# Performance work log

Hardware: AMD Instinct MI355X
Metric: run time of the kernel (lower is better)

The kernel has to match this reference:

```python
import jax, jax.numpy as jnp
import numpy as np

B, K, D = 2048, 100000, 50  # batch, memory-bank size (num users), USER_VEC_DIM

def setup_inputs() -> dict:
    key = jax.random.key(0)
    k1, k2 = jax.random.split(key)
    x = jax.random.normal(k1, (B, D), dtype=jnp.float32)   # batch of user vectors
    M = jax.random.normal(k2, (K, D), dtype=jnp.float32)   # user_memory_vec bank
    return {"x": x, "M": M}

def reference(x, M):
    # Batched form of the per-item Python loop in call():
    #   mu = M @ u ; gamma = softmax(mu, axis=0) ; u_ = sum_k gamma_k * M[k]
    scores = jnp.einsum('bd,kd->bk', x, M)           # [B, K]
    attn = jax.nn.softmax(scores, axis=-1)           # softmax over memory slots
    u_ = jnp.einsum('bk,kd->bd', attn, M)            # attention readout [B, D]
    return jnp.concatenate([x, u_], axis=-1)         # [B, 2D]
```

## Files before the change

kernel.cpp:

```cpp
#include <hip/hip_runtime.h>
#include <hip/hip_bf16.h>
#include <math.h>

#define B_SZ 2048
#define K_SZ 100000
#define D_SZ 50
#define BT   64
#define CK   64
#define STR  72
#define MTS  78
#define SHIFT 30.0f
#define LOG2E 1.4426950408889634f
#define SHIFT_L2 43.280851226668905f
#define PSTRIDE 52
#define NCH   1563
#define IMG_CH 9216
#define IMG_BYTES ((size_t)NCH * IMG_CH * 2)
#define NSEG  18
#define PART_BYTES ((size_t)B_SZ * PSTRIDE * sizeof(float))

typedef short short8 __attribute__((ext_vector_type(8)));
typedef short short4v __attribute__((ext_vector_type(4)));
typedef float f32x4 __attribute__((ext_vector_type(4)));

#if __has_builtin(__builtin_amdgcn_mfma_f32_16x16x16bf16_1k)
#define HAVE_BF16_K16 1
#else
#define HAVE_BF16_K16 0
#endif

__device__ __forceinline__ unsigned short bf16_rne(float f) {
    union { float f; unsigned int u; } v; v.f = f;
    unsigned int r = (v.u + 0x7fffu + ((v.u >> 16) & 1u)) >> 16;
    return (unsigned short)r;
}
__device__ __forceinline__ float bf16_to_f(unsigned short h) {
    union { unsigned int u; float f; } v; v.u = ((unsigned int)h) << 16;
    return v.f;
}

__device__ __forceinline__ void load_lds16(const void* g, void* l) {
    __builtin_amdgcn_global_load_lds(
        (const __attribute__((address_space(1))) unsigned int*)g,
        (__attribute__((address_space(3))) unsigned int*)l, 16, 0, 0);
}

__global__ __launch_bounds__(256)
void precompute_m(const float* __restrict__ M, unsigned short* __restrict__ img) {
    __shared__ __align__(16) unsigned short Mt[64 * MTS];
    const int t = threadIdx.x;
    const int c0 = blockIdx.x;
    const int k0 = c0 * 64;
    for (int i = t; i < (64 * MTS) / 2; i += 256) ((unsigned int*)Mt)[i] = 0;
    __syncthreads();
    unsigned int* gh = (unsigned int*)(img + (size_t)c0 * IMG_CH);
    for (int i = t; i < 64 * 36; i += 256) {
        int r = i / 36, cd = i - r * 36, c = cd * 2;
        int kg = k0 + r;
        unsigned int val = 0;
        if (kg < K_SZ && c < D_SZ) {
            float2 v = *(const float2*)&M[(size_t)kg * D_SZ + c];
            val = ((unsigned int)bf16_rne(v.y) << 16) | bf16_rne(v.x);
            Mt[c * MTS + r]       = (unsigned short)(val & 0xffffu);
            Mt[(c + 1) * MTS + r] = (unsigned short)(val >> 16);
        }
        gh[i] = val;
    }
    __syncthreads();
    unsigned int* gt = (unsigned int*)(img + (size_t)c0 * IMG_CH + 64 * STR);
    for (int i = t; i < 64 * 36; i += 256) {
        int r = i / 36, c = i - r * 36;
        gt[i] = *(const unsigned int*)&Mt[r * MTS + c * 2];
    }
}

__global__ __launch_bounds__(512, 4)
void attend_fast(const float* __restrict__ x, const unsigned short* __restrict__ img,
                 float* __restrict__ part, int slice) {
    __shared__ __align__(16) unsigned short lds[2 * IMG_CH];
    __shared__ float lsc[4][64];

    const int t = threadIdx.x;
    const int w = t >> 6, lane = t & 63;
    const int quad = lane >> 4, lq = lane & 15;

    const int bid = blockIdx.x;
    const int rr = bid >> 3;
    const int split = (rr >> 5) * 8 + (bid & 7);
    const int xtile = rr & 31;
    const int b0 = xtile * BT;
    const int kbeg = split * slice;
    const int kend = min(kbeg + slice, K_SZ);

    const int nt0 = (w & 1) * 2;
    const int mblk = w >> 1;

    short8 xh[2][2], xl[2][2];
    for (int j = 0; j < 2; ++j) {
        int row = b0 + (nt0 + j) * 16 + lq;
        const float* xr = x + (size_t)row * D_SZ;
        for (int ki = 0; ki < 2; ++ki) {
            int d0 = ki * 32 + quad * 8;
            float v[8];
#pragma unroll
            for (int e = 0; e < 8; ++e) v[e] = 0.f;
            if (d0 + 8 <= D_SZ) {
#pragma unroll
                for (int e = 0; e < 4; ++e) {
                    float2 f2 = *(const float2*)&xr[d0 + 2 * e];
                    v[2 * e] = f2.x; v[2 * e + 1] = f2.y;
                }
            } else if (d0 < D_SZ) {
                float2 f2 = *(const float2*)&xr[d0];
                v[0] = f2.x; v[1] = f2.y;
            }
            short8 sh, sl;
#pragma unroll
            for (int e = 0; e < 8; ++e) {
                unsigned short h = bf16_rne(v[e]);
                sh[e] = (short)h;
                sl[e] = (short)bf16_rne(v[e] - bf16_to_f(h));
            }
            xh[j][ki] = sh; xl[j][ki] = sl;
        }
    }

    f32x4 Uacc[2][4] = {};
    float lac[2] = {0.f, 0.f};

    const int ci0 = kbeg >> 6;
    const int nch = (kend - kbeg + CK - 1) / CK;
    const int r0 = bid % nch;

    {
        const unsigned short* g = img + (size_t)(ci0 + r0) * IMG_CH;
        for (int seg = w; seg < NSEG; seg += 8)
            load_lds16((const unsigned int*)(g + seg * 512) + lane * 4, lds + seg * 512);
    }

    for (int i = 0; i < nch; ++i) {
        const int par = i & 1;
        unsigned short* cur = lds + par * IMG_CH;
        unsigned short* nxt = lds + (par ^ 1) * IMG_CH;

        __builtin_amdgcn_s_waitcnt(0);
        __syncthreads();

        if (i + 1 < nch) {
            int cc = r0 + i + 1; if (cc >= nch) cc -= nch;
            const unsigned short* g = img + (size_t)(ci0 + cc) * IMG_CH;
            for (int seg = w; seg < NSEG; seg += 8)
                load_lds16((const unsigned int*)(g + seg * 512) + lane * 4, nxt + seg * 512);
        }

        const unsigned short* Mhi = cur;
        const unsigned short* Mt  = cur + 64 * STR;

        f32x4 S[2] = {};
#pragma unroll
        for (int ki = 0; ki < 2; ++ki) {
            int aoff = (mblk * 16 + lq) * STR + ki * 32 + quad * 8;
            short8 ah = *(const short8*)&Mhi[aoff];
#pragma unroll
            for (int j = 0; j < 2; ++j) {
                S[j] = __builtin_amdgcn_mfma_f32_16x16x32_bf16(ah, xh[j][ki], S[j], 0, 0, 0);
                S[j] = __builtin_amdgcn_mfma_f32_16x16x32_bf16(ah, xl[j][ki], S[j], 0, 0, 0);
            }
        }

#if HAVE_BF16_K16
        short4v pa[2];
#pragma unroll
        for (int j = 0; j < 2; ++j) {
            float p0 = __builtin_amdgcn_exp2f(fmaf(S[j][0], LOG2E, -SHIFT_L2));
            float p1 = __builtin_amdgcn_exp2f(fmaf(S[j][1], LOG2E, -SHIFT_L2));
            float p2 = __builtin_amdgcn_exp2f(fmaf(S[j][2], LOG2E, -SHIFT_L2));
            float p3 = __builtin_amdgcn_exp2f(fmaf(S[j][3], LOG2E, -SHIFT_L2));
            lac[j] += (p0 + p1) + (p2 + p3);
            __hip_bfloat162 q01 = __float22bfloat162_rn(make_float2(p0, p1));
            __hip_bfloat162 q23 = __float22bfloat162_rn(make_float2(p2, p3));
            union { short4v s; unsigned int u[2]; } pk;
            __builtin_memcpy(&pk.u[0], &q01, 4);
            __builtin_memcpy(&pk.u[1], &q23, 4);
            pa[j] = pk.s;
        }

#pragma unroll
        for (int dt = 0; dt < 4; ++dt) {
            short4v bm = *(const short4v*)&Mt[(dt * 16 + lq) * STR + mblk * 16 + quad * 4];
#pragma unroll
            for (int j = 0; j < 2; ++j)
                Uacc[j][dt] = __builtin_amdgcn_mfma_f32_16x16x16bf16_1k(pa[j], bm, Uacc[j][dt], 0, 0, 0);
        }
#else
        short8 pa[2];
#pragma unroll
        for (int j = 0; j < 2; ++j) {
            float p0 = __builtin_amdgcn_exp2f(fmaf(S[j][0], LOG2E, -SHIFT_L2));
            float p1 = __builtin_amdgcn_exp2f(fmaf(S[j][1], LOG2E, -SHIFT_L2));
            float p2 = __builtin_amdgcn_exp2f(fmaf(S[j][2], LOG2E, -SHIFT_L2));
            float p3 = __builtin_amdgcn_exp2f(fmaf(S[j][3], LOG2E, -SHIFT_L2));
            lac[j] += (p0 + p1) + (p2 + p3);
            __hip_bfloat162 q01 = __float22bfloat162_rn(make_float2(p0, p1));
            __hip_bfloat162 q23 = __float22bfloat162_rn(make_float2(p2, p3));
            union { short8 s; unsigned int u[4]; } pk;
            __builtin_memcpy(&pk.u[0], &q01, 4);
            __builtin_memcpy(&pk.u[1], &q23, 4);
            pk.u[2] = 0; pk.u[3] = 0;
            pa[j] = pk.s;
        }
#pragma unroll
        for (int dt = 0; dt < 4; ++dt) {
            short4v b4 = *(const short4v*)&Mt[(dt * 16 + lq) * STR + mblk * 16 + quad * 4];
            short8 b8;
#pragma unroll
            for (int e = 0; e < 4; ++e) { b8[e] = b4[e]; b8[e + 4] = 0; }
#pragma unroll
            for (int j = 0; j < 2; ++j)
                Uacc[j][dt] = __builtin_amdgcn_mfma_f32_16x16x32_bf16(pa[j], b8, Uacc[j][dt], 0, 0, 0);
        }
#endif
    }

    for (int j = 0; j < 2; ++j) {
        float v = lac[j];
        v += __shfl_xor(v, 16);
        v += __shfl_xor(v, 32);
        if (quad == 0) lsc[mblk][(nt0 + j) * 16 + lq] = v;
    }

    float* Ured = (float*)lds;
#pragma unroll
    for (int rnd = 0; rnd < 4; ++rnd) {
        __syncthreads();
        if (mblk == rnd) {
#pragma unroll
            for (int j = 0; j < 2; ++j)
#pragma unroll
                for (int dt = 0; dt < 4; ++dt)
#pragma unroll
                    for (int r4 = 0; r4 < 4; ++r4) {
                        int row = (nt0 + j) * 16 + quad * 4 + r4;
                        int col = dt * 16 + lq;
                        if (rnd == 0) Ured[row * 66 + col] = Uacc[j][dt][r4];
                        else          Ured[row * 66 + col] += Uacc[j][dt][r4];
                    }
        }
    }
    __syncthreads();

    float* pp = part + (size_t)b0 * PSTRIDE;
    for (int i = t; i < BT * D_SZ; i += 512) {
        int row = i / D_SZ, d = i - row * D_SZ;
        atomicAdd(&pp[(size_t)row * PSTRIDE + d], Ured[row * 66 + d]);
    }
    if (t < BT) {
        float Ls = lsc[0][t] + lsc[1][t] + lsc[2][t] + lsc[3][t];
        atomicAdd(&pp[(size_t)t * PSTRIDE + D_SZ], Ls);
    }
}

__global__ __launch_bounds__(512, 4)
void attend_partial_v2(const float* __restrict__ x, const float* __restrict__ M,
                       float* __restrict__ part, int slice) {
    __shared__ __align__(16) unsigned short lds[4 * 64 * STR];
    __shared__ float lsc[4][64];
    unsigned short* bufA  = lds;
    unsigned short* bufB  = lds + 64 * STR;
    unsigned short* Mc_hi = lds + 2 * 64 * STR;
    unsigned short* Mc_lo = lds + 3 * 64 * STR;

    const int t = threadIdx.x;
    const int w = t >> 6, lane = t & 63;
    const int quad = lane >> 4, lq = lane & 15;
    const int b0 = blockIdx.x * 64;
    const int split = blockIdx.y;
    const int kbeg = split * slice;
    const int kend = min(kbeg + slice, K_SZ);

    for (int i = t; i < 4 * 64 * STR; i += 512) lds[i] = 0;
    __syncthreads();
    for (int i = t; i < 64 * 25; i += 512) {
        int r = i / 25, cp = i - r * 25, c = cp * 2;
        float2 v = *(const float2*)&x[(size_t)(b0 + r) * D_SZ + c];
        unsigned short h0 = bf16_rne(v.x), h1 = bf16_rne(v.y);
        unsigned short l0 = bf16_rne(v.x - bf16_to_f(h0));
        unsigned short l1 = bf16_rne(v.y - bf16_to_f(h1));
        *(unsigned int*)&bufA[r * STR + c] = ((unsigned int)h1 << 16) | h0;
        *(unsigned int*)&bufB[r * STR + c] = ((unsigned int)l1 << 16) | l0;
    }
    __syncthreads();

    const int nt0 = (w & 1) * 2;
    const int mblk = w >> 1;
    short8 xh[2][2], xl[2][2];
    for (int j = 0; j < 2; ++j)
        for (int ki = 0; ki < 2; ++ki) {
            int off = ((nt0 + j) * 16 + lq) * STR + ki * 32 + quad * 8;
            xh[j][ki] = *(const short8*)&bufA[off];
            xl[j][ki] = *(const short8*)&bufB[off];
        }

    f32x4 Uacc[2] = {};
    float lac[2] = {0.f, 0.f};

    for (int k0 = kbeg; k0 < kend; k0 += CK) {
        __syncthreads();
        for (int i = t; i < 64 * 25; i += 512) {
            int r = i / 25, cp = i - r * 25, c = cp * 2;
            int kg = k0 + r;
            float2 v = make_float2(0.f, 0.f);
            if (kg < kend) v = *(const float2*)&M[(size_t)kg * D_SZ + c];
            unsigned short h0 = bf16_rne(v.x), h1 = bf16_rne(v.y);
            unsigned short l0 = bf16_rne(v.x - bf16_to_f(h0));
            unsigned short l1 = bf16_rne(v.y - bf16_to_f(h1));
            *(unsigned int*)&Mc_hi[r * STR + c] = ((unsigned int)h1 << 16) | h0;
            *(unsigned int*)&Mc_lo[r * STR + c] = ((unsigned int)l1 << 16) | l0;
            bufB[c * STR + r] = h0;
            bufB[(c + 1) * STR + r] = h1;
        }
        __syncthreads();

        f32x4 S[2] = {};
        for (int ki = 0; ki < 2; ++ki) {
            int aoff = (mblk * 16 + lq) * STR + ki * 32 + quad * 8;
            short8 ah = *(const short8*)&Mc_hi[aoff];
            short8 al = *(const short8*)&Mc_lo[aoff];
            for (int j = 0; j < 2; ++j) {
                S[j] = __builtin_amdgcn_mfma_f32_16x16x32_bf16(ah, xh[j][ki], S[j], 0, 0, 0);
                S[j] = __builtin_amdgcn_mfma_f32_16x16x32_bf16(ah, xl[j][ki], S[j], 0, 0, 0);
                S[j] = __builtin_amdgcn_mfma_f32_16x16x32_bf16(al, xh[j][ki], S[j], 0, 0, 0);
            }
        }
        for (int j = 0; j < 2; ++j) {
            unsigned short pb4[4];
#pragma unroll
            for (int r4 = 0; r4 < 4; ++r4) {
                float p = __expf(S[j][r4] - SHIFT);
                lac[j] += p;
                pb4[r4] = bf16_rne(p);
            }
            int b = (nt0 + j) * 16 + lq;
            int n0 = mblk * 16 + quad * 4;
            *(unsigned int*)&bufA[b * STR + n0]     = ((unsigned int)pb4[1] << 16) | pb4[0];
            *(unsigned int*)&bufA[b * STR + n0 + 2] = ((unsigned int)pb4[3] << 16) | pb4[2];
        }
        __syncthreads();
        for (int ki = 0; ki < 2; ++ki) {
            int poff = (mblk * 16 + lq) * STR + ki * 32 + quad * 8;
            short8 ap = *(const short8*)&bufA[poff];
            for (int j = 0; j < 2; ++j) {
                int doff = ((nt0 + j) * 16 + lq) * STR + ki * 32 + quad * 8;
                short8 bm = *(const short8*)&bufB[doff];
                Uacc[j] = __builtin_amdgcn_mfma_f32_16x16x32_bf16(ap, bm, Uacc[j], 0, 0, 0);
            }
        }
    }

    for (int j = 0; j < 2; ++j) {
        float v = lac[j];
        v += __shfl_xor(v, 16);
        v += __shfl_xor(v, 32);
        if (quad == 0) lsc[mblk][(nt0 + j) * 16 + lq] = v;
    }
    __syncthreads();
    float* pp = part + ((size_t)split * B_SZ + b0) * PSTRIDE;
    for (int j = 0; j < 2; ++j) {
        int d = (nt0 + j) * 16 + lq;
        if (d < D_SZ) {
#pragma unroll
            for (int r4 = 0; r4 < 4; ++r4) {
                int b = mblk * 16 + quad * 4 + r4;
                pp[(size_t)b * PSTRIDE + d] = Uacc[j][r4];
            }
        }
    }
    if (t < 64) {
        float Ls = lsc[0][t] + lsc[1][t] + lsc[2][t] + lsc[3][t];
        pp[(size_t)t * PSTRIDE + D_SZ] = Ls;
    }
}

__global__ __launch_bounds__(256)
void combine_norm(const float* __restrict__ x, const float* __restrict__ part,
                  float* __restrict__ out) {
    const int b = blockIdx.x * 4 + (threadIdx.x >> 6);
    const int t = threadIdx.x & 63;
    if (t < D_SZ) {
        float L = part[(size_t)b * PSTRIDE + D_SZ];
        float acc = part[(size_t)b * PSTRIDE + t];
        out[(size_t)b * (2 * D_SZ) + t] = x[(size_t)b * D_SZ + t];
        out[(size_t)b * (2 * D_SZ) + D_SZ + t] = acc / L;
    }
}

__global__ __launch_bounds__(256)
void combine(const float* __restrict__ x, const float* __restrict__ part,
             float* __restrict__ out, int nsplit) {
    const int b = blockIdx.x * 4 + (threadIdx.x >> 6);
    const int t = threadIdx.x & 63;
    float L = 0.f;
    for (int s = 0; s < nsplit; ++s)
        L += part[((size_t)s * B_SZ + b) * PSTRIDE + D_SZ];
    if (t < D_SZ) {
        float acc = 0.f;
        for (int s = 0; s < nsplit; ++s)
            acc += part[((size_t)s * B_SZ + b) * PSTRIDE + t];
        out[(size_t)b * (2 * D_SZ) + t] = x[(size_t)b * D_SZ + t];
        out[(size_t)b * (2 * D_SZ) + D_SZ + t] = acc / L;
    }
}

extern "C" void kernel_launch(void* const* d_in, const int* in_sizes, int n_in,
                              void* d_out, int out_size, void* d_ws, size_t ws_size,
                              hipStream_t stream) {
    const float* x = (const float*)d_in[0];
    const float* M = (const float*)d_in[1];
    float* out = (float*)d_out;
    const size_t per_split = (size_t)B_SZ * PSTRIDE * sizeof(float);

    if (ws_size >= IMG_BYTES + PART_BYTES) {
        unsigned short* img = (unsigned short*)d_ws;
        float* part = (float*)((char*)d_ws + IMG_BYTES);
        const int ns = 32;
        int slice = (((K_SZ + ns - 1) / ns) + 63) & ~63;
        precompute_m<<<NCH, 256, 0, stream>>>(M, img);
        hipMemsetAsync(part, 0, PART_BYTES, stream);
        attend_fast<<<32 * ns, 512, 0, stream>>>(x, img, part, slice);
        combine_norm<<<B_SZ / 4, 256, 0, stream>>>(x, part, out);
    } else {
        float* part = (float*)d_ws;
        int ns = (int)(ws_size / per_split);
        if (ns > 32) ns = 32;
        if (ns < 1) ns = 1;
        int slice = (K_SZ + ns - 1) / ns;
        dim3 gridA(B_SZ / 64, ns);
        attend_partial_v2<<<gridA, 512, 0, stream>>>(x, M, part, slice);
        combine<<<B_SZ / 4, 256, 0, stream>>>(x, part, out, ns);
    }
}
```

Measured before the change: 181.0 us.

## Replace block-wide LDS double buffer with per-wave swizzled staging and barrier-free pipelining

Each wave now stages only the slice of each M chunk it consumes into its own double-buffered LDS region, using XOR-swizzled global-to-LDS loads. Waits are per-wave vmcnt counts, which removes the block-wide __syncthreads per chunk and prefetches two chunks ahead. The partial-buffer memset is folded into precompute_m, saving one launch, and the slice is rounded to 128. Waves that share an mblk each load the same data separately, which adds redundant global traffic, and the vmcnt-based synchronisation is fragile.

Result: slower. 205.7 us (+13.6%).

```diff
diff --git a/kernel.cpp b/kernel.cpp
--- a/kernel.cpp
+++ b/kernel.cpp
@@ -16,8 +16,8 @@
 #define NCH   1563
 #define IMG_CH 9216
 #define IMG_BYTES ((size_t)NCH * IMG_CH * 2)
-#define NSEG  18
 #define PART_BYTES ((size_t)B_SZ * PSTRIDE * sizeof(float))
+#define WVB 2048
 
 typedef short short8 __attribute__((ext_vector_type(8)));
 typedef short short4v __attribute__((ext_vector_type(4)));
@@ -46,11 +46,13 @@
 }
 
 __global__ __launch_bounds__(256)
-void precompute_m(const float* __restrict__ M, unsigned short* __restrict__ img) {
+void precompute_m(const float* __restrict__ M, unsigned short* __restrict__ img,
+                  float* __restrict__ part) {
     __shared__ __align__(16) unsigned short Mt[64 * MTS];
     const int t = threadIdx.x;
     const int c0 = blockIdx.x;
     const int k0 = c0 * 64;
+    for (int i = c0 * 256 + t; i < B_SZ * PSTRIDE; i += NCH * 256) part[i] = 0.f;
     for (int i = t; i < (64 * MTS) / 2; i += 256) ((unsigned int*)Mt)[i] = 0;
     __syncthreads();
     unsigned int* gh = (unsigned int*)(img + (size_t)c0 * IMG_CH);
@@ -74,10 +76,28 @@
     }
 }
 
+__device__ __forceinline__ void stage_slice(const unsigned short* cbase, int mblk, int lane,
+                                            unsigned short* wbuf) {
+#pragma unroll
+    for (int i = 0; i < 2; ++i) {
+        int slot = i * 64 + lane;
+        int r = slot >> 3, s = slot & 7;
+        const unsigned short* g = cbase + (mblk * 16 + r) * STR + ((s ^ (r & 7)) * 8);
+        load_lds16(g, wbuf + i * 512);
+    }
+#pragma unroll
+    for (int i = 0; i < 2; ++i) {
+        int slot = i * 64 + lane;
+        int rr = slot >> 1, h = slot & 1;
+        const unsigned short* g = cbase + 64 * STR + rr * STR + mblk * 16 + h * 8;
+        load_lds16(g, wbuf + 1024 + i * 512);
+    }
+}
+
 __global__ __launch_bounds__(512, 4)
 void attend_fast(const float* __restrict__ x, const unsigned short* __restrict__ img,
                  float* __restrict__ part, int slice) {
-    __shared__ __align__(16) unsigned short lds[2 * IMG_CH];
+    __shared__ __align__(16) unsigned short stg[8 * 2 * WVB];
     __shared__ float lsc[4][64];
 
     const int t = threadIdx.x;
@@ -130,37 +150,27 @@
 
     const int ci0 = kbeg >> 6;
     const int nch = (kend - kbeg + CK - 1) / CK;
-    const int r0 = bid % nch;
-
-    {
-        const unsigned short* g = img + (size_t)(ci0 + r0) * IMG_CH;
-        for (int seg = w; seg < NSEG; seg += 8)
-            load_lds16((const unsigned int*)(g + seg * 512) + lane * 4, lds + seg * 512);
-    }
-
-    for (int i = 0; i < nch; ++i) {
-        const int par = i & 1;
-        unsigned short* cur = lds + par * IMG_CH;
-        unsigned short* nxt = lds + (par ^ 1) * IMG_CH;
-
-        __builtin_amdgcn_s_waitcnt(0);
-        __syncthreads();
-
-        if (i + 1 < nch) {
-            int cc = r0 + i + 1; if (cc >= nch) cc -= nch;
-            const unsigned short* g = img + (size_t)(ci0 + cc) * IMG_CH;
-            for (int seg = w; seg < NSEG; seg += 8)
-                load_lds16((const unsigned int*)(g + seg * 512) + lane * 4, nxt + seg * 512);
-        }
-
-        const unsigned short* Mhi = cur;
-        const unsigned short* Mt  = cur + 64 * STR;
+    const unsigned short* g0 = img + (size_t)ci0 * IMG_CH;
+
+    unsigned short* wb0 = stg + (w * 2 + 0) * WVB;
+    unsigned short* wb1 = stg + (w * 2 + 1) * WVB;
+
+    stage_slice(g0, mblk, lane, wb0);
+    stage_slice(g0 + IMG_CH, mblk, lane, wb1);
+
+    for (int n = 0; n < nch; ++n) {
+        __builtin_amdgcn_sched_barrier(0);
+        if (n + 1 < nch) asm volatile("s_waitcnt vmcnt(4)" ::: "memory");
+        else             asm volatile("s_waitcnt vmcnt(0)" ::: "memory");
+        __builtin_amdgcn_sched_barrier(0);
+
+        const unsigned short* wb = (n & 1) ? wb1 : wb0;
 
         f32x4 S[2] = {};
 #pragma unroll
         for (int ki = 0; ki < 2; ++ki) {
-            int aoff = (mblk * 16 + lq) * STR + ki * 32 + quad * 8;
-            short8 ah = *(const short8*)&Mhi[aoff];
+            int sidx = (ki * 4 + quad) ^ (lq & 7);
+            short8 ah = *(const short8*)&wb[lq * 64 + sidx * 8];
 #pragma unroll
             for (int j = 0; j < 2; ++j) {
                 S[j] = __builtin_amdgcn_mfma_f32_16x16x32_bf16(ah, xh[j][ki], S[j], 0, 0, 0);
@@ -184,10 +194,9 @@
             __builtin_memcpy(&pk.u[1], &q23, 4);
             pa[j] = pk.s;
         }
-
 #pragma unroll
         for (int dt = 0; dt < 4; ++dt) {
-            short4v bm = *(const short4v*)&Mt[(dt * 16 + lq) * STR + mblk * 16 + quad * 4];
+            short4v bm = *(const short4v*)&wb[1024 + (dt * 16 + lq) * 16 + quad * 4];
 #pragma unroll
             for (int j = 0; j < 2; ++j)
                 Uacc[j][dt] = __builtin_amdgcn_mfma_f32_16x16x16bf16_1k(pa[j], bm, Uacc[j][dt], 0, 0, 0);
@@ -211,7 +220,7 @@
         }
 #pragma unroll
         for (int dt = 0; dt < 4; ++dt) {
-            short4v b4 = *(const short4v*)&Mt[(dt * 16 + lq) * STR + mblk * 16 + quad * 4];
+            short4v b4 = *(const short4v*)&wb[1024 + (dt * 16 + lq) * 16 + quad * 4];
             short8 b8;
 #pragma unroll
             for (int e = 0; e < 4; ++e) { b8[e] = b4[e]; b8[e + 4] = 0; }
@@ -220,6 +229,11 @@
                 Uacc[j][dt] = __builtin_amdgcn_mfma_f32_16x16x32_bf16(pa[j], b8, Uacc[j][dt], 0, 0, 0);
         }
 #endif
+
+        if (n + 2 < nch) {
+            __builtin_amdgcn_sched_barrier(0);
+            stage_slice(g0 + (size_t)(n + 2) * IMG_CH, mblk, lane, (n & 1) ? wb1 : wb0);
+        }
     }
 
     for (int j = 0; j < 2; ++j) {
@@ -229,7 +243,7 @@
         if (quad == 0) lsc[mblk][(nt0 + j) * 16 + lq] = v;
     }
 
-    float* Ured = (float*)lds;
+    float* Ured = (float*)stg;
 #pragma unroll
     for (int rnd = 0; rnd < 4; ++rnd) {
         __syncthreads();
@@ -423,9 +437,8 @@
         unsigned short* img = (unsigned short*)d_ws;
         float* part = (float*)((char*)d_ws + IMG_BYTES);
         const int ns = 32;
-        int slice = (((K_SZ + ns - 1) / ns) + 63) & ~63;
-        precompute_m<<<NCH, 256, 0, stream>>>(M, img);
-        hipMemsetAsync(part, 0, PART_BYTES, stream);
+        int slice = (((K_SZ + ns - 1) / ns) + 127) & ~127;
+        precompute_m<<<NCH, 256, 0, stream>>>(M, img, part);
         attend_fast<<<32 * ns, 512, 0, stream>>>(x, img, part, slice);
         combine_norm<<<B_SZ / 4, 256, 0, stream>>>(x, part, out);
     } else {
```
